# Optimization experiments

Hardware: AMD Instinct MI355X
Metric: run time of the kernel (lower is better)

The kernel has to match this reference:

```python
import jax, jax.numpy as jnp
import numpy as np

B, N_ATOMS = 64, 127            # graphs, atoms per graph (uniform)
L = N_ATOMS + 1                 # +1 cls token
D_MODEL, NHEAD, NUM_LAYERS, D_FF = 1024, 16, 8, 3072
HEAD_DIM = D_MODEL // NHEAD
MAX_TOKENS = 131                # 121 + 10
NEIGH_VOCAB = 14 + 3            # max_neighbors + 3
DIST_VOCAB = 83 + 3             # max_distance + 3
EPS = 1e-5


def _dist_bins():
    # short_cutoff=0.9, long_cutoff=5.0, precision=0.05; first 3 edges overridden
    b = np.arange(0.9 - 3 * 0.05, 5.0, 0.05)
    b[:3] = [-1.0, 0.0, 0.01]
    return jnp.asarray(b, jnp.float32)  # len 85 -> digitize indices in [0, 85]


def _layer_norm(x, g, b):
    m = jnp.mean(x, -1, keepdims=True)
    v = jnp.var(x, -1, keepdims=True)
    return (x - m) * jax.lax.rsqrt(v + EPS) * g + b


def setup_inputs() -> dict:
    key = jax.random.key(0)
    ks = jax.random.split(key, 16)
    s = 0.02
    z = jax.random.randint(ks[0], (B * N_ATOMS,), 0, 119)
    hgs = jax.random.randint(ks[1], (B * N_ATOMS,), 0, 15)
    pos = jax.random.normal(ks[2], (B * N_ATOMS, 3), jnp.float32) * 3.0
    batch = jnp.repeat(jnp.arange(B, dtype=jnp.int64), N_ATOMS)
    atoms_emb = (jax.random.normal(ks[3], (MAX_TOKENS, D_MODEL), jnp.float32) * s).at[0].set(0.0)  # padding_idx=0
    neigh_emb = (jax.random.normal(ks[4], (NEIGH_VOCAB, D_MODEL), jnp.float32) * s).at[0].set(0.0)
    dist_emb = jax.random.normal(ks[5], (DIST_VOCAB, NHEAD), jnp.float32) * s  # row 0 forced to -inf in reference
    Wqkv = jax.random.normal(ks[6], (D_MODEL, 3 * D_MODEL), jnp.float32) * s
    bqkv = jnp.zeros((3 * D_MODEL,), jnp.float32)
    Wo = jax.random.normal(ks[7], (D_MODEL, D_MODEL), jnp.float32) * s
    bo = jnp.zeros((D_MODEL,), jnp.float32)
    W1 = jax.random.normal(ks[8], (D_MODEL, D_FF), jnp.float32) * s
    b1f = jnp.zeros((D_FF,), jnp.float32)
    W2 = jax.random.normal(ks[9], (D_FF, D_MODEL), jnp.float32) * s
    b2f = jnp.zeros((D_MODEL,), jnp.float32)
    ln1_g = jnp.ones((D_MODEL,), jnp.float32); ln1_b = jnp.zeros((D_MODEL,), jnp.float32)
    ln2_g = jnp.ones((D_MODEL,), jnp.float32); ln2_b = jnp.zeros((D_MODEL,), jnp.float32)
    return dict(z=z, hgs=hgs, pos=pos, batch=batch, atoms_emb=atoms_emb, neigh_emb=neigh_emb,
                dist_emb=dist_emb, Wqkv=Wqkv, bqkv=bqkv, Wo=Wo, bo=bo,
                W1=W1, b1f=b1f, W2=W2, b2f=b2f,
                ln1_g=ln1_g, ln1_b=ln1_b, ln2_g=ln2_g, ln2_b=ln2_b)


def reference(z, hgs, pos, batch, atoms_emb, neigh_emb, dist_emb,
              Wqkv, bqkv, Wo, bo, W1, b1f, W2, b2f, ln1_g, ln1_b, ln2_g, ln2_b):
    # batch is uniform (N_ATOMS per graph, sorted), so per-graph batching == reshape
    zb = z.reshape(B, N_ATOMS).astype(jnp.int32) + 2
    hb = hgs.reshape(B, N_ATOMS).astype(jnp.int32) + 2
    atoms = jnp.concatenate([jnp.ones((B, 1), jnp.int32), zb], axis=1)        # cls token = 1
    neighbors = jnp.concatenate([jnp.zeros((B, 1), jnp.int32), hb], axis=1)   # cls neighbors = 0

    p = pos.reshape(B, N_ATOMS, 3)
    dist = jnp.sqrt(jnp.sum((p[:, None, :, :] - p[:, :, None, :]) ** 2, axis=-1))  # (B,n,n)
    didx = jnp.digitize(dist, _dist_bins()).astype(jnp.int32)                      # self-loop -> 2
    distances = jnp.ones((B, L, L), jnp.int32).at[:, 1:, 1:].set(didx)             # cls row/col = 1

    # neg_inf_idx=0 padding mask row (unused here since no padding -> indices >= 1)
    w_d = dist_emb.at[0].set(-jnp.inf)
    d_mask = w_d[distances].transpose(0, 3, 1, 2)  # (B, H, L, L)

    x = atoms_emb[atoms] + neigh_emb[neighbors]    # (B, L, D)
    scale = 1.0 / jnp.sqrt(jnp.float32(HEAD_DIM))
    for _ in range(NUM_LAYERS):  # shared weights + shared attention bias
        qkv = x @ Wqkv + bqkv
        q, k, v = jnp.split(qkv, 3, axis=-1)
        q = q.reshape(B, L, NHEAD, HEAD_DIM)
        k = k.reshape(B, L, NHEAD, HEAD_DIM)
        v = v.reshape(B, L, NHEAD, HEAD_DIM)
        scores = jnp.einsum('blhd,bmhd->bhlm', q, k) * scale + d_mask
        a = jax.nn.softmax(scores, axis=-1)
        o = jnp.einsum('bhlm,bmhd->blhd', a, v).reshape(B, L, D_MODEL) @ Wo + bo
        x = _layer_norm(x + o, ln1_g, ln1_b)                      # post-norm (norm_first=False)
        h = jax.nn.gelu(x @ W1 + b1f, approximate=False) @ W2 + b2f
        x = _layer_norm(x + h, ln2_g, ln2_b)
    return x[:, 0]  # cls embedding, (B, D_MODEL)
```

## Files before the change

kernel.cpp:

```cpp
#include <hip/hip_runtime.h>
#include <cstdint>
#include <math.h>

typedef unsigned short u16;
typedef __attribute__((ext_vector_type(4))) float f32x4;
typedef __attribute__((ext_vector_type(8))) __bf16 bf16x8;
typedef __attribute__((ext_vector_type(8))) short short8;

typedef __attribute__((address_space(1))) void g_void;
typedef __attribute__((address_space(3))) void l_void;

__device__ __forceinline__ u16 f2bf(float f) {
  uint32_t u = __builtin_bit_cast(uint32_t, f);
  u += 0x7FFFu + ((u >> 16) & 1u);
  return (u16)(u >> 16);
}
__device__ __forceinline__ float bf2f(u16 h) {
  uint32_t u = ((uint32_t)h) << 16;
  return __builtin_bit_cast(float, u);
}

__device__ __forceinline__ void gload16(const void* g, void* l) {
  __builtin_amdgcn_global_load_lds((g_void*)g, (l_void*)l, 16, 0, 0);
}

__device__ __forceinline__ float gelu_exact(float x) {
  float a = x * 0.70710678118654752f;
  float s = fabsf(a);
  float t = __builtin_amdgcn_rcpf(fmaf(0.3275911f, s, 1.0f));
  float p = fmaf(fmaf(fmaf(fmaf(1.061405429f, t, -1.453152027f), t, 1.421413741f), t,
                      -0.284496736f), t, 0.254829592f);
  p *= t;
  float e = __expf(-s * s);
  float er = fmaf(-p, e, 1.0f);
  er = copysignf(er, a);
  return 0.5f * x * (1.0f + er);
}

__global__ void transpose_w(const float* __restrict__ W, u16* __restrict__ Wt, int K, int N) {
  __shared__ float t[32][33];
  const int nb = blockIdx.x * 32, kb = blockIdx.y * 32;
  const int tx = threadIdx.x, ty = threadIdx.y;
#pragma unroll
  for (int i = 0; i < 32; i += 8)
    t[ty + i][tx] = W[(size_t)(kb + ty + i) * N + nb + tx];
  __syncthreads();
#pragma unroll
  for (int i = 0; i < 32; i += 8)
    Wt[(size_t)(nb + ty + i) * K + kb + tx] = f2bf(t[tx][ty + i]);
}

__global__ void embed_k(const int* __restrict__ z, const int* __restrict__ hgs,
                        const float* __restrict__ ae, const float* __restrict__ ne,
                        u16* __restrict__ xb) {
  const int row = blockIdx.x;
  const int b = row >> 7, tl = row & 127;
  int ia = 1, in_ = 0;
  if (tl > 0) { ia = z[b * 127 + tl - 1] + 2; in_ = hgs[b * 127 + tl - 1] + 2; }
  const float* ar = ae + (size_t)ia * 1024;
  const float* nr = ne + (size_t)in_ * 1024;
  for (int c = threadIdx.x; c < 1024; c += 256)
    xb[(size_t)row * 1024 + c] = f2bf(ar[c] + nr[c]);
}

__global__ void mask_k(const float* __restrict__ pos, const float* __restrict__ demb,
                       u16* __restrict__ mask) {
  __shared__ float edges[85];
  __shared__ float dh[86 * 16];
  const int bq = blockIdx.x;
  const int b = bq >> 7, lq = bq & 127;
  const int lk = threadIdx.x;
  if (lk < 85) {
    double e = 0.75 + 0.05 * (double)lk;
    float ef = (float)e;
    if (lk == 0) ef = -1.0f; else if (lk == 1) ef = 0.0f; else if (lk == 2) ef = 0.01f;
    edges[lk] = ef;
  }
  for (int i = lk; i < 86 * 16; i += 128) {
    float v = demb[i];
    if (i < 16) v = -INFINITY;
    dh[i] = v;
  }
  __syncthreads();
  int c;
  if (lq == 0 || lk == 0) {
    c = 1;
  } else {
    const float* pi = pos + ((size_t)b * 127 + lq - 1) * 3;
    const float* pj = pos + ((size_t)b * 127 + lk - 1) * 3;
    const float dx = pi[0] - pj[0], dy = pi[1] - pj[1], dz = pi[2] - pj[2];
    const float d = sqrtf(dx * dx + dy * dy + dz * dz);
    int cnt = 0;
#pragma unroll
    for (int k2 = 0; k2 < 85; ++k2) cnt += (edges[k2] <= d) ? 1 : 0;
    c = cnt;
  }
#pragma unroll
  for (int h = 0; h < 16; ++h)
    mask[(((size_t)b * 16 + h) * 128 + lq) * 128 + lk] = f2bf(dh[c * 16 + h]);
}

template <int MODE>
__launch_bounds__(512, 4)
__global__ void gemmS(const u16* __restrict__ A, const u16* __restrict__ Bt,
                      const float* __restrict__ bias,
                      u16* __restrict__ O0, u16* __restrict__ O1, u16* __restrict__ O2,
                      float* __restrict__ Pout,
                      int N, int K, int ntiles, int kLen) {
  extern __shared__ char lds[];
  constexpr int SLAB = 24576;
  const int tid = threadIdx.x;
  const int w = tid >> 6, l = tid & 63;
  const int wr = w >> 1, wc = w & 1;
  const int nwg = gridDim.x;
  const int wg = (blockIdx.x & 7) * (nwg >> 3) + (blockIdx.x >> 3);
  const int s = wg / ntiles;
  const int tile = wg - s * ntiles;
  const int ntn = N >> 7;
  const int bm = tile / ntn, bn = tile - (tile / ntn) * ntn;
  const int kStart = s * kLen;
  const int NT = kLen >> 5;

  const int colc = ((((l & 3) << 4) ^ (((l >> 2) & 8) << 2)) >> 1);
  const u16* Ag = A + (size_t)(bm * 256 + w * 16 + (l >> 2)) * K + kStart + colc;
  const u16* Bg = Bt + (size_t)(bn * 128 + w * 16 + (l >> 2)) * K + kStart + colc;
  const int ldst = w << 10;

  auto stage = [&](int t, char* buf) {
    const int kb = t << 5;
    gload16(Ag + kb, buf + ldst);
    gload16(Ag + (size_t)128 * K + kb, buf + 8192 + ldst);
    gload16(Bg + kb, buf + 16384 + ldst);
  };

  const int lo = ((l & 15) << 6) + (((l >> 4) << 4) ^ ((l & 8) << 2));

  f32x4 acc[4][4];
#pragma unroll
  for (int m = 0; m < 4; ++m)
#pragma unroll
    for (int n = 0; n < 4; ++n) acc[m][n] = f32x4{0.f, 0.f, 0.f, 0.f};

  char* p0 = lds;
  char* p1 = lds + SLAB;
  char* p2 = lds + 2 * SLAB;

  stage(0, p0);
  stage(1, p1);
  asm volatile("s_waitcnt vmcnt(3)" ::: "memory");
  __builtin_amdgcn_s_barrier();

  for (int t = 0; t < NT; ++t) {
    if (t + 2 < NT) stage(t + 2, p2);
    const char* ab = p0 + (wr << 12);
    const char* bb = p0 + 16384 + (wc << 12);
    bf16x8 af[4], bf[4];
#pragma unroll
    for (int m = 0; m < 4; ++m) af[m] = *(const bf16x8*)(ab + (m << 10) + lo);
#pragma unroll
    for (int n = 0; n < 4; ++n) bf[n] = *(const bf16x8*)(bb + (n << 10) + lo);
    __builtin_amdgcn_s_setprio(1);
#pragma unroll
    for (int m = 0; m < 4; ++m)
#pragma unroll
      for (int n = 0; n < 4; ++n)
        acc[m][n] = __builtin_amdgcn_mfma_f32_16x16x32_bf16(af[m], bf[n], acc[m][n], 0, 0, 0);
    __builtin_amdgcn_s_setprio(0);
    if (t + 2 < NT) asm volatile("s_waitcnt vmcnt(3)" ::: "memory");
    else            asm volatile("s_waitcnt vmcnt(0)" ::: "memory");
    __builtin_amdgcn_s_barrier();
    char* tmp = p0; p0 = p1; p1 = p2; p2 = tmp;
  }

  const int fr = l & 15, fq = l >> 4;
  const int colb = bn * 128 + wc * 64;
  const int rowb = bm * 256 + wr * 64;
  float bv[4];
  if (MODE != 3) {
#pragma unroll
    for (int n = 0; n < 4; ++n) bv[n] = bias[colb + n * 16 + fr];
  }
  const int region = colb >> 10;

#pragma unroll
  for (int m = 0; m < 4; ++m) {
#pragma unroll
    for (int n = 0; n < 4; ++n) {
      const int col = colb + n * 16 + fr;
      if (MODE == 0 && region == 2) {
        const int row0_ = rowb + m * 16 + fq * 4;
        const int bI = row0_ >> 7, tl0 = row0_ & 127;
        const int c = col & 1023, h = c >> 6, d = c & 63;
        ushort4 pk;
        pk.x = f2bf(acc[m][n][0] + bv[n]);
        pk.y = f2bf(acc[m][n][1] + bv[n]);
        pk.z = f2bf(acc[m][n][2] + bv[n]);
        pk.w = f2bf(acc[m][n][3] + bv[n]);
        *(ushort4*)&O2[(((size_t)bI * 16 + h) * 64 + d) * 128 + tl0] = pk;
      } else {
#pragma unroll
        for (int j = 0; j < 4; ++j) {
          const int row = rowb + m * 16 + fq * 4 + j;
          if (MODE == 3) {
            Pout[(size_t)s * 8388608 + (size_t)row * N + col] = acc[m][n][j];
          } else {
            float v = acc[m][n][j] + bv[n];
            if (MODE == 2) v = gelu_exact(v);
            if (MODE == 0) {
              const int bI = row >> 7, tl = row & 127;
              const int c = col & 1023, h = c >> 6, d = c & 63;
              if (region == 0) O0[(((size_t)bI * 16 + h) * 128 + tl) * 64 + d] = f2bf(v);
              else             O1[(((size_t)bI * 16 + h) * 128 + tl) * 64 + d] = f2bf(v);
            } else {
              O0[(size_t)row * N + col] = f2bf(v);
            }
          }
        }
      }
    }
  }
}

__launch_bounds__(256)
__global__ void attn_kernel(const u16* __restrict__ Qg, const u16* __restrict__ Kg,
                            const u16* __restrict__ Vg,
                            const u16* __restrict__ mask,
                            u16* __restrict__ Og) {
  __shared__ u16 QK[2 * 128 * 64];
  __shared__ u16 Vt[64 * 128];
  const int tid = threadIdx.x;
  const int wv = tid >> 6;
  const int l = tid & 63;
  const int bh = blockIdx.x;
  const int b = bh >> 4;

  const char* Qs = (const char*)(Qg + (size_t)bh * 8192);
  const char* Ks = (const char*)(Kg + (size_t)bh * 8192);
  const char* Vs = (const char*)(Vg + (size_t)bh * 8192);
  char* QKb = (char*)QK;
  char* Vtb = (char*)Vt;
#pragma unroll
  for (int it = 0; it < 4; ++it) {
    const int r = it * 32 + (tid >> 3);
    const int cb = (tid & 7) * 16;
    const int sw = cb ^ ((r & 7) << 4);
    *(uint4*)(QKb + r * 128 + sw) = *(const uint4*)(Qs + r * 128 + cb);
    *(uint4*)(QKb + 16384 + r * 128 + sw) = *(const uint4*)(Ks + r * 128 + cb);
  }
#pragma unroll
  for (int it = 0; it < 4; ++it) {
    const int r = it * 16 + (tid >> 4);
    const int cb = (tid & 15) * 16;
    const int sw = cb ^ ((r & 7) << 4);
    *(uint4*)(Vtb + r * 256 + sw) = *(const uint4*)(Vs + r * 256 + cb);
  }
  __syncthreads();

  f32x4 s[2][8];
#pragma unroll
  for (int m = 0; m < 2; ++m)
#pragma unroll
    for (int n = 0; n < 8; ++n) s[m][n] = f32x4{0.f, 0.f, 0.f, 0.f};
#pragma unroll
  for (int kk = 0; kk < 2; ++kk) {
    bf16x8 qa[2], kb[8];
#pragma unroll
    for (int m = 0; m < 2; ++m) {
      const int qr = wv * 32 + m * 16 + (l & 15);
      qa[m] = *(const bf16x8*)(QKb + qr * 128 + ((kk * 64 + (l >> 4) * 16) ^ ((qr & 7) << 4)));
    }
#pragma unroll
    for (int n = 0; n < 8; ++n) {
      const int kr = n * 16 + (l & 15);
      kb[n] = *(const bf16x8*)(QKb + 16384 + kr * 128 + ((kk * 64 + (l >> 4) * 16) ^ ((kr & 7) << 4)));
    }
#pragma unroll
    for (int m = 0; m < 2; ++m)
#pragma unroll
      for (int n = 0; n < 8; ++n)
        s[m][n] = __builtin_amdgcn_mfma_f32_16x16x32_bf16(qa[m], kb[n], s[m][n], 0, 0, 0);
  }

  const u16* mbase = mask + (size_t)bh * 16384;
  float rinv[2][4];
#pragma unroll
  for (int m = 0; m < 2; ++m) {
#pragma unroll
    for (int j = 0; j < 4; ++j) {
      const int lq = wv * 32 + m * 16 + (l >> 4) * 4 + j;
      const u16* mrow = mbase + lq * 128 + (l & 15);
      float vals[8];
#pragma unroll
      for (int n = 0; n < 8; ++n)
        vals[n] = fmaf(s[m][n][j], 0.125f, bf2f(mrow[n * 16]));
      float mx = vals[0];
#pragma unroll
      for (int n = 1; n < 8; ++n) mx = fmaxf(mx, vals[n]);
#pragma unroll
      for (int o = 1; o < 16; o <<= 1) mx = fmaxf(mx, __shfl_xor(mx, o, 64));
      float sum = 0.f;
#pragma unroll
      for (int n = 0; n < 8; ++n) { vals[n] = expf(vals[n] - mx); sum += vals[n]; }
#pragma unroll
      for (int o = 1; o < 16; o <<= 1) sum += __shfl_xor(sum, o, 64);
      rinv[m][j] = 1.f / sum;
#pragma unroll
      for (int n = 0; n < 8; ++n) s[m][n][j] = vals[n];
    }
  }
  __syncthreads();
  char* Pb = QKb + wv * 8192;
#pragma unroll
  for (int m = 0; m < 2; ++m)
#pragma unroll
    for (int n = 0; n < 8; ++n)
#pragma unroll
      for (int j = 0; j < 4; ++j) {
        const int pr = m * 16 + (l >> 4) * 4 + j;
        const int pc = (n * 16 + (l & 15)) * 2;
        *(u16*)(Pb + pr * 256 + (pc ^ ((pr & 7) << 4))) = f2bf(s[m][n][j]);
      }
  __syncthreads();

  f32x4 o_[2][4];
#pragma unroll
  for (int m = 0; m < 2; ++m)
#pragma unroll
    for (int n = 0; n < 4; ++n) o_[m][n] = f32x4{0.f, 0.f, 0.f, 0.f};
#pragma unroll
  for (int ks = 0; ks < 4; ++ks) {
    bf16x8 pa[2], vb[4];
#pragma unroll
    for (int m = 0; m < 2; ++m) {
      const int pr = m * 16 + (l & 15);
      pa[m] = *(const bf16x8*)(Pb + pr * 256 + ((ks * 64 + (l >> 4) * 16) ^ ((pr & 7) << 4)));
    }
#pragma unroll
    for (int n = 0; n < 4; ++n) {
      const int vr = n * 16 + (l & 15);
      vb[n] = *(const bf16x8*)(Vtb + vr * 256 + ((ks * 64 + (l >> 4) * 16) ^ ((vr & 7) << 4)));
    }
#pragma unroll
    for (int m = 0; m < 2; ++m)
#pragma unroll
      for (int n = 0; n < 4; ++n)
        o_[m][n] = __builtin_amdgcn_mfma_f32_16x16x32_bf16(pa[m], vb[n], o_[m][n], 0, 0, 0);
  }
  const int h = bh & 15;
#pragma unroll
  for (int m = 0; m < 2; ++m)
#pragma unroll
    for (int n = 0; n < 4; ++n)
#pragma unroll
      for (int j = 0; j < 4; ++j) {
        const int lo2 = wv * 32 + m * 16 + (l >> 4) * 4 + j;
        const int d = n * 16 + (l & 15);
        Og[((size_t)b * 128 + lo2) * 1024 + h * 64 + d] = f2bf(o_[m][n][j] * rinv[m][j]);
      }
}

__launch_bounds__(256)
__global__ void ln_resS(u16* __restrict__ xb, const float* __restrict__ P,
                        const float* __restrict__ bias,
                        const float* __restrict__ gam, const float* __restrict__ bet,
                        float* __restrict__ cls_out) {
  const int row = blockIdx.x * 4 + (threadIdx.x >> 6);
  const int l = threadIdx.x & 63;
  const size_t base = (size_t)row * 1024 + l * 16;
  const int c0 = l * 16;
  float v[16], gv[16], bb[16], bi[16], pa[16], pb[16];
  const short8 xa = *(const short8*)(xb + base);
  const short8 xc = *(const short8*)(xb + base + 8);
#pragma unroll
  for (int i = 0; i < 4; ++i) {
    *(float4*)&pa[i * 4] = *(const float4*)(P + base + i * 4);
    *(float4*)&pb[i * 4] = *(const float4*)(P + 8388608 + base + i * 4);
    *(float4*)&gv[i * 4] = *(const float4*)(gam + c0 + i * 4);
    *(float4*)&bb[i * 4] = *(const float4*)(bet + c0 + i * 4);
    *(float4*)&bi[i * 4] = *(const float4*)(bias + c0 + i * 4);
  }
  float s = 0.f, sq = 0.f;
#pragma unroll
  for (int i = 0; i < 8; ++i) {
    v[i] = bf2f((u16)xa[i]) + pa[i] + pb[i] + bi[i];
    v[i + 8] = bf2f((u16)xc[i]) + pa[i + 8] + pb[i + 8] + bi[i + 8];
  }
#pragma unroll
  for (int i = 0; i < 16; ++i) { s += v[i]; sq += v[i] * v[i]; }
#pragma unroll
  for (int off = 1; off < 64; off <<= 1) {
    s += __shfl_xor(s, off, 64);
    sq += __shfl_xor(sq, off, 64);
  }
  const float mean = s * (1.f / 1024.f);
  const float var = sq * (1.f / 1024.f) - mean * mean;
  const float rstd = rsqrtf(var + 1e-5f);
  short8 ra, rc;
#pragma unroll
  for (int i = 0; i < 8; ++i) {
    const float ya = (v[i] - mean) * rstd * gv[i] + bb[i];
    const float yc = (v[i + 8] - mean) * rstd * gv[i + 8] + bb[i + 8];
    ra[i] = (short)f2bf(ya);
    rc[i] = (short)f2bf(yc);
    if ((row & 127) == 0) {
      cls_out[(size_t)(row >> 7) * 1024 + c0 + i] = ya;
      cls_out[(size_t)(row >> 7) * 1024 + c0 + 8 + i] = yc;
    }
  }
  *(short8*)(xb + base) = ra;
  *(short8*)(xb + base + 8) = rc;
}

extern "C" void kernel_launch(void* const* d_in, const int* in_sizes, int n_in,
                              void* d_out, int out_size, void* d_ws, size_t ws_size,
                              hipStream_t stream) {
  const int* z = (const int*)d_in[0];
  const int* hgs = (const int*)d_in[1];
  const float* pos = (const float*)d_in[2];
  const float* atoms_emb = (const float*)d_in[4];
  const float* neigh_emb = (const float*)d_in[5];
  const float* dist_emb = (const float*)d_in[6];
  const float* Wqkv = (const float*)d_in[7];
  const float* bqkv = (const float*)d_in[8];
  const float* Wo = (const float*)d_in[9];
  const float* bo = (const float*)d_in[10];
  const float* W1 = (const float*)d_in[11];
  const float* b1f = (const float*)d_in[12];
  const float* W2 = (const float*)d_in[13];
  const float* b2f = (const float*)d_in[14];
  const float* ln1g = (const float*)d_in[15];
  const float* ln1b = (const float*)d_in[16];
  const float* ln2g = (const float*)d_in[17];
  const float* ln2b = (const float*)d_in[18];

  size_t off = 0;
  char* wsb = (char*)d_ws;
  auto alc = [&](size_t bytes) { void* p = wsb + off; off += (bytes + 255) & ~(size_t)255; return p; };
  u16* xb = (u16*)alc(8192ull * 1024 * 2);
  u16* q = (u16*)alc(8192ull * 1024 * 2);
  u16* k = (u16*)alc(8192ull * 1024 * 2);
  u16* v = (u16*)alc(8192ull * 1024 * 2);
  u16* proj = (u16*)alc(8192ull * 1024 * 2);
  u16* big = (u16*)alc(8192ull * 3072 * 2);
  u16* wqkvt = (u16*)alc(3072ull * 1024 * 2);
  u16* wot = (u16*)alc(1024ull * 1024 * 2);
  u16* w1t = (u16*)alc(3072ull * 1024 * 2);
  u16* w2t = (u16*)alc(1024ull * 3072 * 2);
  u16* mask = (u16*)alc(64ull * 16 * 128 * 128 * 2);
  float* pp = (float*)q;
  (void)proj;

  hipFuncSetAttribute((const void*)gemmS<0>, hipFuncAttributeMaxDynamicSharedMemorySize, 73728);
  hipFuncSetAttribute((const void*)gemmS<2>, hipFuncAttributeMaxDynamicSharedMemorySize, 73728);
  hipFuncSetAttribute((const void*)gemmS<3>, hipFuncAttributeMaxDynamicSharedMemorySize, 73728);

  transpose_w<<<dim3(96, 32), dim3(32, 8), 0, stream>>>(Wqkv, wqkvt, 1024, 3072);
  transpose_w<<<dim3(32, 32), dim3(32, 8), 0, stream>>>(Wo, wot, 1024, 1024);
  transpose_w<<<dim3(96, 32), dim3(32, 8), 0, stream>>>(W1, w1t, 1024, 3072);
  transpose_w<<<dim3(32, 96), dim3(32, 8), 0, stream>>>(W2, w2t, 3072, 1024);
  embed_k<<<8192, 256, 0, stream>>>(z, hgs, atoms_emb, neigh_emb, xb);
  mask_k<<<8192, 128, 0, stream>>>(pos, dist_emb, mask);

  float* cls = (float*)d_out;
  for (int layer = 0; layer < 8; ++layer) {
    gemmS<0><<<768, 512, 73728, stream>>>(xb, wqkvt, bqkv, q, k, v, nullptr, 3072, 1024, 768, 1024);
    attn_kernel<<<1024, 256, 0, stream>>>(q, k, v, mask, big);
    gemmS<3><<<512, 512, 73728, stream>>>(big, wot, nullptr, nullptr, nullptr, nullptr, pp, 1024, 1024, 256, 512);
    ln_resS<<<2048, 256, 0, stream>>>(xb, pp, bo, ln1g, ln1b, cls);
    gemmS<2><<<768, 512, 73728, stream>>>(xb, w1t, b1f, big, nullptr, nullptr, nullptr, 3072, 1024, 768, 1024);
    gemmS<3><<<512, 512, 73728, stream>>>(big, w2t, nullptr, nullptr, nullptr, nullptr, pp, 1024, 3072, 256, 1536);
    ln_resS<<<2048, 256, 0, stream>>>(xb, pp, b2f, ln2g, ln2b, cls);
  }
}
```

Before: 2.315 ms.

## Replace split-K fp32 partial GEMMs with 128x128 tile GEMM and pre-permuted mask layout

The Wo and W2 projections no longer use split-K with two fp32 partial buffers. They now run a dedicated 128x128-tile GEMM (256 threads) that adds the bias and writes bf16 output directly, so the LayerNorm kernel reads one bf16 tensor instead of two fp32 partials plus the bias. This cuts memory traffic in both the GEMM epilogue and the LayerNorm, at the cost of a full-K loop per tile with no split. The attention mask is also stored in a permuted layout so each lane loads its 8 mask values with one 16-byte vector load instead of 8 strided scalar loads.

After: 2.211 ms. 1.05x faster.

```diff
diff --git a/kernel.cpp b/kernel.cpp
--- a/kernel.cpp
+++ b/kernel.cpp
@@ -95,9 +95,10 @@
     for (int k2 = 0; k2 < 85; ++k2) cnt += (edges[k2] <= d) ? 1 : 0;
     c = cnt;
   }
+  const int fr = lk & 15, nn = lk >> 4;
 #pragma unroll
   for (int h = 0; h < 16; ++h)
-    mask[(((size_t)b * 16 + h) * 128 + lq) * 128 + lk] = f2bf(dh[c * 16 + h]);
+    mask[((((size_t)(b * 16 + h) * 16 + fr) * 128 + lq) << 3) + nn] = f2bf(dh[c * 16 + h]);
 }
 
 template <int MODE>
@@ -105,8 +106,7 @@
 __global__ void gemmS(const u16* __restrict__ A, const u16* __restrict__ Bt,
                       const float* __restrict__ bias,
                       u16* __restrict__ O0, u16* __restrict__ O1, u16* __restrict__ O2,
-                      float* __restrict__ Pout,
-                      int N, int K, int ntiles, int kLen) {
+                      int N, int K) {
   extern __shared__ char lds[];
   constexpr int SLAB = 24576;
   const int tid = threadIdx.x;
@@ -114,16 +114,13 @@
   const int wr = w >> 1, wc = w & 1;
   const int nwg = gridDim.x;
   const int wg = (blockIdx.x & 7) * (nwg >> 3) + (blockIdx.x >> 3);
-  const int s = wg / ntiles;
-  const int tile = wg - s * ntiles;
   const int ntn = N >> 7;
-  const int bm = tile / ntn, bn = tile - (tile / ntn) * ntn;
-  const int kStart = s * kLen;
-  const int NT = kLen >> 5;
+  const int bm = wg / ntn, bn = wg - (wg / ntn) * ntn;
+  const int NT = K >> 5;
 
   const int colc = ((((l & 3) << 4) ^ (((l >> 2) & 8) << 2)) >> 1);
-  const u16* Ag = A + (size_t)(bm * 256 + w * 16 + (l >> 2)) * K + kStart + colc;
-  const u16* Bg = Bt + (size_t)(bn * 128 + w * 16 + (l >> 2)) * K + kStart + colc;
+  const u16* Ag = A + (size_t)(bm * 256 + w * 16 + (l >> 2)) * K + colc;
+  const u16* Bg = Bt + (size_t)(bn * 128 + w * 16 + (l >> 2)) * K + colc;
   const int ldst = w << 10;
 
   auto stage = [&](int t, char* buf) {
@@ -176,10 +173,8 @@
   const int colb = bn * 128 + wc * 64;
   const int rowb = bm * 256 + wr * 64;
   float bv[4];
-  if (MODE != 3) {
-#pragma unroll
-    for (int n = 0; n < 4; ++n) bv[n] = bias[colb + n * 16 + fr];
-  }
+#pragma unroll
+  for (int n = 0; n < 4; ++n) bv[n] = bias[colb + n * 16 + fr];
   const int region = colb >> 10;
 
 #pragma unroll
@@ -201,24 +196,106 @@
 #pragma unroll
         for (int j = 0; j < 4; ++j) {
           const int row = rowb + m * 16 + fq * 4 + j;
-          if (MODE == 3) {
-            Pout[(size_t)s * 8388608 + (size_t)row * N + col] = acc[m][n][j];
+          float v = acc[m][n][j] + bv[n];
+          if (MODE == 2) v = gelu_exact(v);
+          if (MODE == 0) {
+            const int bI = row >> 7, tl = row & 127;
+            const int c = col & 1023, h = c >> 6, d = c & 63;
+            if (region == 0) O0[(((size_t)bI * 16 + h) * 128 + tl) * 64 + d] = f2bf(v);
+            else             O1[(((size_t)bI * 16 + h) * 128 + tl) * 64 + d] = f2bf(v);
           } else {
-            float v = acc[m][n][j] + bv[n];
-            if (MODE == 2) v = gelu_exact(v);
-            if (MODE == 0) {
-              const int bI = row >> 7, tl = row & 127;
-              const int c = col & 1023, h = c >> 6, d = c & 63;
-              if (region == 0) O0[(((size_t)bI * 16 + h) * 128 + tl) * 64 + d] = f2bf(v);
-              else             O1[(((size_t)bI * 16 + h) * 128 + tl) * 64 + d] = f2bf(v);
-            } else {
-              O0[(size_t)row * N + col] = f2bf(v);
-            }
+            O0[(size_t)row * N + col] = f2bf(v);
           }
         }
       }
     }
   }
+}
+
+__launch_bounds__(256, 3)
+__global__ void gemm4(const u16* __restrict__ A, const u16* __restrict__ Bt,
+                      const float* __restrict__ bias, u16* __restrict__ O,
+                      int N, int K) {
+  extern __shared__ char lds[];
+  constexpr int SLAB = 16384;
+  const int tid = threadIdx.x;
+  const int w = tid >> 6, l = tid & 63;
+  const int wr = w >> 1, wc = w & 1;
+  const int nwg = gridDim.x;
+  const int wg = (blockIdx.x & 7) * (nwg >> 3) + (blockIdx.x >> 3);
+  const int ntn = N >> 7;
+  const int bm = wg / ntn, bn = wg - (wg / ntn) * ntn;
+  const int NT = K >> 5;
+
+  const int colc = ((((l & 3) << 4) ^ (((l >> 2) & 8) << 2)) >> 1);
+  const u16* Ag = A + (size_t)(bm * 128 + w * 16 + (l >> 2)) * K + colc;
+  const u16* Bg = Bt + (size_t)(bn * 128 + w * 16 + (l >> 2)) * K + colc;
+  const int ldst = w << 10;
+
+  auto stage = [&](int t, char* buf) {
+    const int kb = t << 5;
+    gload16(Ag + kb, buf + ldst);
+    gload16(Ag + (size_t)64 * K + kb, buf + 4096 + ldst);
+    gload16(Bg + kb, buf + 8192 + ldst);
+    gload16(Bg + (size_t)64 * K + kb, buf + 12288 + ldst);
+  };
+
+  const int lo = ((l & 15) << 6) + (((l >> 4) << 4) ^ ((l & 8) << 2));
+
+  f32x4 acc[4][4];
+#pragma unroll
+  for (int m = 0; m < 4; ++m)
+#pragma unroll
+    for (int n = 0; n < 4; ++n) acc[m][n] = f32x4{0.f, 0.f, 0.f, 0.f};
+
+  char* p0 = lds;
+  char* p1 = lds + SLAB;
+  char* p2 = lds + 2 * SLAB;
+
+  stage(0, p0);
+  stage(1, p1);
+  asm volatile("s_waitcnt vmcnt(4)" ::: "memory");
+  __builtin_amdgcn_s_barrier();
+
+  for (int t = 0; t < NT; ++t) {
+    if (t + 2 < NT) stage(t + 2, p2);
+    const char* ab = p0 + (wr << 12);
+    const char* bb = p0 + 8192 + (wc << 12);
+    bf16x8 af[4], bf[4];
+#pragma unroll
+    for (int m = 0; m < 4; ++m) af[m] = *(const bf16x8*)(ab + (m << 10) + lo);
+#pragma unroll
+    for (int n = 0; n < 4; ++n) bf[n] = *(const bf16x8*)(bb + (n << 10) + lo);
+    __builtin_amdgcn_s_setprio(1);
+#pragma unroll
+    for (int m = 0; m < 4; ++m)
+#pragma unroll
+      for (int n = 0; n < 4; ++n)
+        acc[m][n] = __builtin_amdgcn_mfma_f32_16x16x32_bf16(af[m], bf[n], acc[m][n], 0, 0, 0);
+    __builtin_amdgcn_s_setprio(0);
+    if (t + 2 < NT) asm volatile("s_waitcnt vmcnt(4)" ::: "memory");
+    else            asm volatile("s_waitcnt vmcnt(0)" ::: "memory");
+    __builtin_amdgcn_s_barrier();
+    char* tmp = p0; p0 = p1; p1 = p2; p2 = tmp;
+  }
+
+  const int fr = l & 15, fq = l >> 4;
+  const int colb = bn * 128 + wc * 64;
+  const int rowb = bm * 128 + wr * 64;
+  float bv[4];
+#pragma unroll
+  for (int n = 0; n < 4; ++n) bv[n] = bias[colb + n * 16 + fr];
+#pragma unroll
+  for (int m = 0; m < 4; ++m)
+#pragma unroll
+    for (int n = 0; n < 4; ++n) {
+      const int col = colb + n * 16 + fr;
+#pragma unroll
+      for (int j = 0; j < 4; ++j) {
+        const int row = rowb + m * 16 + fq * 4 + j;
+        O[(size_t)row * N + col] = f2bf(acc[m][n][j] + bv[n]);
+      }
+    }
 }
 
 __launch_bounds__(256)
@@ -281,18 +358,18 @@
         s[m][n] = __builtin_amdgcn_mfma_f32_16x16x32_bf16(qa[m], kb[n], s[m][n], 0, 0, 0);
   }
 
-  const u16* mbase = mask + (size_t)bh * 16384;
+  const u16* mb2 = mask + (((size_t)bh * 16 + (l & 15)) << 10);
   float rinv[2][4];
 #pragma unroll
   for (int m = 0; m < 2; ++m) {
 #pragma unroll
     for (int j = 0; j < 4; ++j) {
       const int lq = wv * 32 + m * 16 + (l >> 4) * 4 + j;
-      const u16* mrow = mbase + lq * 128 + (l & 15);
+      const short8 mv = *(const short8*)(mb2 + lq * 8);
       float vals[8];
 #pragma unroll
       for (int n = 0; n < 8; ++n)
-        vals[n] = fmaf(s[m][n][j], 0.125f, bf2f(mrow[n * 16]));
+        vals[n] = fmaf(s[m][n][j], 0.125f, bf2f((u16)mv[n]));
       float mx = vals[0];
 #pragma unroll
       for (int n = 1; n < 8; ++n) mx = fmaxf(mx, vals[n]);
@@ -360,30 +437,28 @@
 }
 
 __launch_bounds__(256)
-__global__ void ln_resS(u16* __restrict__ xb, const float* __restrict__ P,
-                        const float* __restrict__ bias,
-                        const float* __restrict__ gam, const float* __restrict__ bet,
-                        float* __restrict__ cls_out) {
+__global__ void ln_res(u16* __restrict__ xb, const u16* __restrict__ o,
+                       const float* __restrict__ gam, const float* __restrict__ bet,
+                       float* __restrict__ cls_out) {
   const int row = blockIdx.x * 4 + (threadIdx.x >> 6);
   const int l = threadIdx.x & 63;
   const size_t base = (size_t)row * 1024 + l * 16;
   const int c0 = l * 16;
-  float v[16], gv[16], bb[16], bi[16], pa[16], pb[16];
+  float v[16], gv[16], bb[16];
   const short8 xa = *(const short8*)(xb + base);
   const short8 xc = *(const short8*)(xb + base + 8);
+  const short8 oa = *(const short8*)(o + base);
+  const short8 oc = *(const short8*)(o + base + 8);
 #pragma unroll
   for (int i = 0; i < 4; ++i) {
-    *(float4*)&pa[i * 4] = *(const float4*)(P + base + i * 4);
-    *(float4*)&pb[i * 4] = *(const float4*)(P + 8388608 + base + i * 4);
     *(float4*)&gv[i * 4] = *(const float4*)(gam + c0 + i * 4);
     *(float4*)&bb[i * 4] = *(const float4*)(bet + c0 + i * 4);
-    *(float4*)&bi[i * 4] = *(const float4*)(bias + c0 + i * 4);
   }
   float s = 0.f, sq = 0.f;
 #pragma unroll
   for (int i = 0; i < 8; ++i) {
-    v[i] = bf2f((u16)xa[i]) + pa[i] + pb[i] + bi[i];
-    v[i + 8] = bf2f((u16)xc[i]) + pa[i + 8] + pb[i + 8] + bi[i + 8];
+    v[i] = bf2f((u16)xa[i]) + bf2f((u16)oa[i]);
+    v[i + 8] = bf2f((u16)xc[i]) + bf2f((u16)oc[i]);
   }
 #pragma unroll
   for (int i = 0; i < 16; ++i) { s += v[i]; sq += v[i] * v[i]; }
@@ -446,13 +521,11 @@
   u16* wot = (u16*)alc(1024ull * 1024 * 2);
   u16* w1t = (u16*)alc(3072ull * 1024 * 2);
   u16* w2t = (u16*)alc(1024ull * 3072 * 2);
-  u16* mask = (u16*)alc(64ull * 16 * 128 * 128 * 2);
-  float* pp = (float*)q;
-  (void)proj;
+  u16* mask = (u16*)alc(64ull * 16 * 16 * 128 * 8 * 2);
 
   hipFuncSetAttribute((const void*)gemmS<0>, hipFuncAttributeMaxDynamicSharedMemorySize, 73728);
   hipFuncSetAttribute((const void*)gemmS<2>, hipFuncAttributeMaxDynamicSharedMemorySize, 73728);
-  hipFuncSetAttribute((const void*)gemmS<3>, hipFuncAttributeMaxDynamicSharedMemorySize, 73728);
+  hipFuncSetAttribute((const void*)gemm4, hipFuncAttributeMaxDynamicSharedMemorySize, 49152);
 
   transpose_w<<<dim3(96, 32), dim3(32, 8), 0, stream>>>(Wqkv, wqkvt, 1024, 3072);
   transpose_w<<<dim3(32, 32), dim3(32, 8), 0, stream>>>(Wo, wot, 1024, 1024);
@@ -463,12 +536,12 @@
 
   float* cls = (float*)d_out;
   for (int layer = 0; layer < 8; ++layer) {
-    gemmS<0><<<768, 512, 73728, stream>>>(xb, wqkvt, bqkv, q, k, v, nullptr, 3072, 1024, 768, 1024);
+    gemmS<0><<<768, 512, 73728, stream>>>(xb, wqkvt, bqkv, q, k, v, 3072, 1024);
     attn_kernel<<<1024, 256, 0, stream>>>(q, k, v, mask, big);
-    gemmS<3><<<512, 512, 73728, stream>>>(big, wot, nullptr, nullptr, nullptr, nullptr, pp, 1024, 1024, 256, 512);
-    ln_resS<<<2048, 256, 0, stream>>>(xb, pp, bo, ln1g, ln1b, cls);
-    gemmS<2><<<768, 512, 73728, stream>>>(xb, w1t, b1f, big, nullptr, nullptr, nullptr, 3072, 1024, 768, 1024);
-    gemmS<3><<<512, 512, 73728, stream>>>(big, w2t, nullptr, nullptr, nullptr, nullptr, pp, 1024, 3072, 256, 1536);
-    ln_resS<<<2048, 256, 0, stream>>>(xb, pp, b2f, ln2g, ln2b, cls);
-  }
-}
+    gemm4<<<512, 256, 49152, stream>>>(big, wot, bo, proj, 1024, 1024);
+    ln_res<<<2048, 256, 0, stream>>>(xb, proj, ln1g, ln1b, cls);
+    gemmS<2><<<768, 512, 73728, stream>>>(xb, w1t, b1f, big, nullptr, nullptr, 3072, 1024);
+    gemm4<<<512, 256, 49152, stream>>>(big, w2t, b2f, proj, 1024, 3072);
+    ln_res<<<2048, 256, 0, stream>>>(xb, proj, ln2g, ln2b, cls);
+  }
+}
```
